# Performance work log

Hardware: AMD Instinct MI355X
Metric: run time of the kernel (lower is better)

Reference implementation:

```python
import jax, jax.numpy as jnp
import numpy as np

IN_DIM = 8192
OUT_DIM = 8192
BATCH = 2048


def setup_inputs() -> dict:
    key = jax.random.key(0)
    k1, k2, k3, k4 = jax.random.split(key, 4)
    x = jax.random.uniform(k1, (BATCH, IN_DIM), dtype=jnp.float32)  # soft bits in [0,1]
    weights = jax.random.normal(k2, (OUT_DIM, 16), dtype=jnp.float32)
    idx_a = jax.random.randint(k3, (OUT_DIM,), 0, IN_DIM, dtype=jnp.int64)
    idx_b = jax.random.randint(k4, (OUT_DIM,), 0, IN_DIM, dtype=jnp.int64)
    return {"x": x, "weights": weights, "idx_a": idx_a, "idx_b": idx_b}


def _gate_values(a, b):
    # The 16 real-valued relaxations of the 2-input binary logic gates.
    ab = a * b
    return [
        jnp.zeros_like(a),      # 0:  False
        ab,                     # 1:  a AND b
        a - ab,                 # 2:  a AND NOT b
        a,                      # 3:  a
        b - ab,                 # 4:  NOT a AND b
        b,                      # 5:  b
        a + b - 2.0 * ab,       # 6:  a XOR b
        a + b - ab,             # 7:  a OR b
        1.0 - (a + b - ab),     # 8:  NOT (a OR b)
        1.0 - (a + b - 2.0 * ab),  # 9: NOT (a XOR b)
        1.0 - b,                # 10: NOT b
        1.0 - b + ab,           # 11: a OR NOT b
        1.0 - a,                # 12: NOT a
        1.0 - a + ab,           # 13: NOT a OR b
        1.0 - ab,               # 14: NOT (a AND b)
        jnp.ones_like(a),       # 15: True
    ]


def reference(x, weights, idx_a, idx_b):
    # training=True path of LogicLayer.forward_python
    a = x[:, idx_a]  # [B, OUT]
    b = x[:, idx_b]  # [B, OUT]
    w = jax.nn.softmax(weights, axis=-1)  # [OUT, 16]
    gates = _gate_values(a, b)
    out = jnp.zeros_like(a)
    for k in range(16):  # fixed small structural loop over the 16 gates
        out = out + w[None, :, k] * gates[k]
    return out
```

## Files before the change

### kernel.cpp

```cpp
#include <hip/hip_runtime.h>

#define IN_DIM 8192
#define OUT_DIM 8192
#define BATCH 2048
#define TPB 512
#define JITER (OUT_DIM / 4 / TPB)

typedef float fvec4 __attribute__((ext_vector_type(4)));

__global__ __launch_bounds__(256) void coeff_kernel(
    const float* __restrict__ w,
    float* __restrict__ c0, float* __restrict__ ca,
    float* __restrict__ cb, float* __restrict__ cab)
{
    int j = blockIdx.x * blockDim.x + threadIdx.x;
    if (j >= OUT_DIM) return;

    const float* wj = w + (size_t)j * 16;
    float wv[16];
    float m = -1e30f;
#pragma unroll
    for (int k = 0; k < 16; ++k) { wv[k] = wj[k]; m = fmaxf(m, wv[k]); }
    float s = 0.f;
#pragma unroll
    for (int k = 0; k < 16; ++k) { wv[k] = __expf(wv[k] - m); s += wv[k]; }
    float inv = 1.0f / s;
#pragma unroll
    for (int k = 0; k < 16; ++k) wv[k] *= inv;

    c0[j]  = wv[8] + wv[9] + wv[10] + wv[11] + wv[12] + wv[13] + wv[14] + wv[15];
    ca[j]  = wv[2] + wv[3] + wv[6] + wv[7] - wv[8] - wv[9] - wv[12] - wv[13];
    cb[j]  = wv[4] + wv[5] + wv[6] + wv[7] - wv[8] - wv[9] - wv[10] - wv[11];
    cab[j] = wv[1] - wv[2] - wv[4] - 2.f * wv[6] - wv[7]
           + wv[8] + 2.f * wv[9] + wv[11] + wv[13] - wv[14];
}

__global__ __launch_bounds__(TPB) void logic_kernel(
    const float* __restrict__ x,
    const int* __restrict__ idx_a,
    const int* __restrict__ idx_b,
    const float* __restrict__ c0, const float* __restrict__ ca,
    const float* __restrict__ cb, const float* __restrict__ cab,
    float* __restrict__ out)
{
    __shared__ float xrow[IN_DIM];

    const int i = blockIdx.x;
    const float4* xr4 = (const float4*)(x + (size_t)i * IN_DIM);
    float4* xs4 = (float4*)xrow;
#pragma unroll
    for (int k = 0; k < IN_DIM / 4 / TPB; ++k) {
        int idx = k * TPB + threadIdx.x;
        xs4[idx] = xr4[idx];
    }

    const int4*   ia4  = (const int4*)idx_a;
    const int4*   ib4  = (const int4*)idx_b;
    const float4* c04  = (const float4*)c0;
    const float4* ca4  = (const float4*)ca;
    const float4* cb4  = (const float4*)cb;
    const float4* cab4 = (const float4*)cab;
    fvec4* out4 = (fvec4*)(out + (size_t)i * OUT_DIM);

    int4   ia[JITER], ib[JITER];
    float4 v0[JITER], va[JITER], vb[JITER], vab[JITER];
#pragma unroll
    for (int it = 0; it < JITER; ++it) {
        int j4 = it * TPB + threadIdx.x;
        ia[it]  = ia4[j4];
        ib[it]  = ib4[j4];
        v0[it]  = c04[j4];
        va[it]  = ca4[j4];
        vb[it]  = cb4[j4];
        vab[it] = cab4[j4];
    }

    __syncthreads();

#pragma unroll
    for (int it = 0; it < JITER; ++it) {
        int j4 = it * TPB + threadIdx.x;

        float a0 = xrow[ia[it].x], b0 = xrow[ib[it].x];
        float a1 = xrow[ia[it].y], b1 = xrow[ib[it].y];
        float a2 = xrow[ia[it].z], b2 = xrow[ib[it].z];
        float a3 = xrow[ia[it].w], b3 = xrow[ib[it].w];

        fvec4 o;
        o.x = v0[it].x + va[it].x * a0 + vb[it].x * b0 + vab[it].x * (a0 * b0);
        o.y = v0[it].y + va[it].y * a1 + vb[it].y * b1 + vab[it].y * (a1 * b1);
        o.z = v0[it].z + va[it].z * a2 + vb[it].z * b2 + vab[it].z * (a2 * b2);
        o.w = v0[it].w + va[it].w * a3 + vb[it].w * b3 + vab[it].w * (a3 * b3);
        __builtin_nontemporal_store(o, &out4[j4]);
    }
}

extern "C" void kernel_launch(void* const* d_in, const int* in_sizes, int n_in,
                              void* d_out, int out_size, void* d_ws, size_t ws_size,
                              hipStream_t stream)
{
    const float* x       = (const float*)d_in[0];
    const float* weights = (const float*)d_in[1];
    const int*   idx_a   = (const int*)d_in[2];
    const int*   idx_b   = (const int*)d_in[3];
    float* out = (float*)d_out;

    float* wsF = (float*)d_ws;
    float* c0  = wsF;
    float* ca  = wsF + OUT_DIM;
    float* cb  = wsF + 2 * OUT_DIM;
    float* cab = wsF + 3 * OUT_DIM;

    coeff_kernel<<<OUT_DIM / 256, 256, 0, stream>>>(weights, c0, ca, cb, cab);
    logic_kernel<<<BATCH, TPB, 0, stream>>>(x, idx_a, idx_b, c0, ca, cb, cab, out);
}
```

Baseline: 123.8 us.

## Process multiple rows per block with double-buffered LDS and register prefetch

Each block now handles 8 batch rows over half the output columns, double-buffering the x row in shared memory and prefetching the next row into registers while computing the current one. Index and coefficient loads are amortized across the rows, and a lighter custom barrier replaces __syncthreads. This reduces per-row setup traffic and overlaps global loads with gather/compute, but doubles x reads (two column tiles) and cuts the grid to 512 blocks, which may reduce parallelism. There is one barrier per row, so the buffer being refilled may not be protected against readers still working on the row from two iterations earlier.

After: 129.2 us. 4.4% more time.

```diff
diff --git a/kernel.cpp b/kernel.cpp
--- a/kernel.cpp
+++ b/kernel.cpp
@@ -3,10 +3,17 @@
 #define IN_DIM 8192
 #define OUT_DIM 8192
 #define BATCH 2048
+
 #define TPB 512
-#define JITER (OUT_DIM / 4 / TPB)
+#define JT 2
+#define JTILE (OUT_DIM / JT)
+#define OPT (JTILE / TPB / 4)
+#define RROWS 8
+#define SVEC (IN_DIM / 4 / TPB)
 
 typedef float fvec4 __attribute__((ext_vector_type(4)));
+
+#define BAR() __asm__ __volatile__("s_waitcnt lgkmcnt(0)\n\ts_barrier" ::: "memory")
 
 __global__ __launch_bounds__(256) void coeff_kernel(
     const float* __restrict__ w,
@@ -35,7 +42,7 @@
            + wv[8] + 2.f * wv[9] + wv[11] + wv[13] - wv[14];
 }
 
-__global__ __launch_bounds__(TPB) void logic_kernel(
+__global__ __launch_bounds__(TPB, 4) void logic_kernel(
     const float* __restrict__ x,
     const int* __restrict__ idx_a,
     const int* __restrict__ idx_b,
@@ -43,16 +50,13 @@
     const float* __restrict__ cb, const float* __restrict__ cab,
     float* __restrict__ out)
 {
-    __shared__ float xrow[IN_DIM];
+    __shared__ float xrow[2][IN_DIM];
 
-    const int i = blockIdx.x;
-    const float4* xr4 = (const float4*)(x + (size_t)i * IN_DIM);
-    float4* xs4 = (float4*)xrow;
-#pragma unroll
-    for (int k = 0; k < IN_DIM / 4 / TPB; ++k) {
-        int idx = k * TPB + threadIdx.x;
-        xs4[idx] = xr4[idx];
-    }
+    const int jt    = blockIdx.x & (JT - 1);
+    const int rg    = blockIdx.x / JT;
+    const int row0  = rg * RROWS;
+    const int jb4   = jt * (JTILE / 4);
+    const int tid   = threadIdx.x;
 
     const int4*   ia4  = (const int4*)idx_a;
     const int4*   ib4  = (const int4*)idx_b;
@@ -60,13 +64,12 @@
     const float4* ca4  = (const float4*)ca;
     const float4* cb4  = (const float4*)cb;
     const float4* cab4 = (const float4*)cab;
-    fvec4* out4 = (fvec4*)(out + (size_t)i * OUT_DIM);
 
-    int4   ia[JITER], ib[JITER];
-    float4 v0[JITER], va[JITER], vb[JITER], vab[JITER];
+    int4   ia[OPT], ib[OPT];
+    float4 v0[OPT], va[OPT], vb[OPT], vab[OPT];
 #pragma unroll
-    for (int it = 0; it < JITER; ++it) {
-        int j4 = it * TPB + threadIdx.x;
+    for (int it = 0; it < OPT; ++it) {
+        int j4  = jb4 + it * TPB + tid;
         ia[it]  = ia4[j4];
         ib[it]  = ib4[j4];
         v0[it]  = c04[j4];
@@ -75,23 +78,44 @@
         vab[it] = cab4[j4];
     }
 
-    __syncthreads();
+    float4 pf[SVEC];
+    {
+        const float4* xr4 = (const float4*)(x + (size_t)row0 * IN_DIM);
+#pragma unroll
+        for (int k = 0; k < SVEC; ++k) pf[k] = xr4[k * TPB + tid];
+    }
 
+    for (int r = 0; r < RROWS; ++r) {
+        float4* buf4 = (float4*)xrow[r & 1];
 #pragma unroll
-    for (int it = 0; it < JITER; ++it) {
-        int j4 = it * TPB + threadIdx.x;
+        for (int k = 0; k < SVEC; ++k) buf4[k * TPB + tid] = pf[k];
 
-        float a0 = xrow[ia[it].x], b0 = xrow[ib[it].x];
-        float a1 = xrow[ia[it].y], b1 = xrow[ib[it].y];
-        float a2 = xrow[ia[it].z], b2 = xrow[ib[it].z];
-        float a3 = xrow[ia[it].w], b3 = xrow[ib[it].w];
+        if (r + 1 < RROWS) {
+            const float4* xr4 = (const float4*)(x + (size_t)(row0 + r + 1) * IN_DIM);
+#pragma unroll
+            for (int k = 0; k < SVEC; ++k) pf[k] = xr4[k * TPB + tid];
+        }
 
-        fvec4 o;
-        o.x = v0[it].x + va[it].x * a0 + vb[it].x * b0 + vab[it].x * (a0 * b0);
-        o.y = v0[it].y + va[it].y * a1 + vb[it].y * b1 + vab[it].y * (a1 * b1);
-        o.z = v0[it].z + va[it].z * a2 + vb[it].z * b2 + vab[it].z * (a2 * b2);
-        o.w = v0[it].w + va[it].w * a3 + vb[it].w * b3 + vab[it].w * (a3 * b3);
-        __builtin_nontemporal_store(o, &out4[j4]);
+        BAR();
+
+        const float* xr = xrow[r & 1];
+        fvec4* out4 = (fvec4*)(out + (size_t)(row0 + r) * OUT_DIM);
+#pragma unroll
+        for (int it = 0; it < OPT; ++it) {
+            int j4 = jb4 + it * TPB + tid;
+
+            float a0 = xr[ia[it].x], b0 = xr[ib[it].x];
+            float a1 = xr[ia[it].y], b1 = xr[ib[it].y];
+            float a2 = xr[ia[it].z], b2 = xr[ib[it].z];
+            float a3 = xr[ia[it].w], b3 = xr[ib[it].w];
+
+            fvec4 o;
+            o.x = v0[it].x + va[it].x * a0 + vb[it].x * b0 + vab[it].x * (a0 * b0);
+            o.y = v0[it].y + va[it].y * a1 + vb[it].y * b1 + vab[it].y * (a1 * b1);
+            o.z = v0[it].z + va[it].z * a2 + vb[it].z * b2 + vab[it].z * (a2 * b2);
+            o.w = v0[it].w + va[it].w * a3 + vb[it].w * b3 + vab[it].w * (a3 * b3);
+            __builtin_nontemporal_store(o, &out4[j4]);
+        }
     }
 }
 
@@ -112,5 +136,6 @@
     float* cab = wsF + 3 * OUT_DIM;
 
     coeff_kernel<<<OUT_DIM / 256, 256, 0, stream>>>(weights, c0, ca, cb, cab);
-    logic_kernel<<<BATCH, TPB, 0, stream>>>(x, idx_a, idx_b, c0, ca, cb, cab, out);
+    logic_kernel<<<JT * (BATCH / RROWS), TPB, 0, stream>>>(
+        x, idx_a, idx_b, c0, ca, cb, cab, out);
 }
```
